# Performance work log

Hardware: AMD Instinct MI355X
Metric: run time of the kernel (lower is better)

The kernel has to match this reference:

```python
import jax, jax.numpy as jnp
import numpy as np

DIM = 1024
HEADS = 16
HEAD_DIM = DIM // HEADS


def rotate_half(x):
    x1, x2 = jnp.split(x, 2, axis=-1)
    return jnp.concatenate((-x2, x1), axis=-1)


def rope_tables(T, D, dtype=jnp.float32):
    inv_freq = 1.0 / (10000.0 ** (jnp.arange(0, D, 2, dtype=jnp.float32) / D))
    t = jnp.arange(T, dtype=jnp.float32)
    freqs = jnp.einsum('i,j->ij', t, inv_freq)  # [T, D/2]
    emb = jnp.concatenate((freqs, freqs), axis=-1)  # [T, D]
    return emb.astype(dtype), jnp.cos(emb).astype(dtype), jnp.sin(emb).astype(dtype)


def setup_inputs() -> dict:
    key = jax.random.key(0)
    kx, kq, kk, kv, ko = jax.random.split(key, 5)
    B, T = 2, 4096
    scale = 1.0 / np.sqrt(DIM)
    x = jax.random.normal(kx, (B, T, DIM), dtype=jnp.float32)
    wq = jax.random.normal(kq, (DIM, DIM), dtype=jnp.float32) * scale
    wk = jax.random.normal(kk, (DIM, DIM), dtype=jnp.float32) * scale
    wv = jax.random.normal(kv, (DIM, DIM), dtype=jnp.float32) * scale
    wo = jax.random.normal(ko, (DIM, DIM), dtype=jnp.float32) * scale
    return {"x": x, "wq": wq, "wk": wk, "wv": wv, "wo": wo}


def reference(x, wq, wk, wv, wo):
    B, T, C = x.shape
    H, D = HEADS, HEAD_DIM
    # projections; nn.Linear applies x @ W^T
    q = (x @ wq.T).reshape(B, T, H, D).transpose(0, 2, 1, 3)  # [B,H,T,D]
    k = (x @ wk.T).reshape(B, T, H, D).transpose(0, 2, 1, 3)
    v = (x @ wv.T).reshape(B, T, H, D).transpose(0, 2, 1, 3)
    _, cos, sin = rope_tables(T, D, x.dtype)
    cos = cos[None, None]  # [1,1,T,D]
    sin = sin[None, None]
    q = q * cos + rotate_half(q) * sin
    k = k * cos + rotate_half(k) * sin
    scores = jnp.einsum('bhtd,bhsd->bhts', q, k) / jnp.sqrt(jnp.asarray(D, x.dtype))
    attn = jax.nn.softmax(scores, axis=-1)
    out = jnp.einsum('bhts,bhsd->bhtd', attn, v)
    out = out.transpose(0, 2, 1, 3).reshape(B, T, C)
    return out @ wo.T
```

## Files before the change

### kernel.cpp

```cpp
#include <hip/hip_runtime.h>
#include <hip/hip_bf16.h>
#include <math.h>


typedef __attribute__((ext_vector_type(8))) short short8;
typedef __attribute__((ext_vector_type(4))) short short4v;
typedef __attribute__((ext_vector_type(4))) float floatx4;

using bf16 = __hip_bfloat16;

static constexpr int T_ = 4096;
static constexpr int C_ = 1024;
static constexpr int M_ = 8192;
static constexpr float QSCALE = 0.125f * 1.44269504088896340736f;

#if __has_builtin(__builtin_amdgcn_mfma_f32_16x16x16bf16_1k)
#define USE_K16 1
#else
#define USE_K16 0
#endif

#if __has_builtin(__builtin_amdgcn_exp2f)
#define EXP2 __builtin_amdgcn_exp2f
#else
#define EXP2 exp2f
#endif

__device__ __forceinline__ floatx4 mfma16(short8 a, short8 b, floatx4 c) {
    return __builtin_amdgcn_mfma_f32_16x16x32_bf16(a, b, c, 0, 0, 0);
}
#if USE_K16
__device__ __forceinline__ floatx4 mfma_k16(short4v a, short4v b, floatx4 c) {
    return __builtin_amdgcn_mfma_f32_16x16x16bf16_1k(a, b, c, 0, 0, 0);
}
#endif

__device__ __forceinline__ short8 ld8(const bf16* p) {
    return *reinterpret_cast<const short8*>(p);
}
__device__ __forceinline__ short4v ld4(const bf16* p) {
    return *reinterpret_cast<const short4v*>(p);
}
__device__ __forceinline__ void st8(bf16* p, short8 v) {
    *reinterpret_cast<short8*>(p) = v;
}
__device__ __forceinline__ unsigned short f2bf(float x) {
    bf16 h = __float2bfloat16(x);
    return reinterpret_cast<unsigned short&>(h);
}

__device__ __forceinline__ int pack2bf(float a, float b) {
    const unsigned ua = (__float_as_uint(a) + 0x8000u) >> 16;
    const unsigned ub = (__float_as_uint(b) + 0x8000u) & 0xFFFF0000u;
    return (int)(ua | ub);
}
__device__ __forceinline__ short4v i2s4(int lo, int hi) {
    union { int2 i; short4v s; } u;
    u.i.x = lo; u.i.y = hi;
    return u.s;
}

__device__ __forceinline__ void cp16(const bf16* g, bf16* l) {
    __builtin_amdgcn_global_load_lds(
        (const __attribute__((address_space(1))) void*)g,
        (__attribute__((address_space(3))) void*)l, 16, 0, 0);
}

__global__ __launch_bounds__(256)
void cvt_kernel(const float* __restrict__ in, bf16* __restrict__ out, int n8) {
    const int i = blockIdx.x * blockDim.x + threadIdx.x;
    if (i >= n8) return;
    const float4* p = reinterpret_cast<const float4*>(in) + (size_t)i * 2;
    const float4 a = p[0];
    const float4 b = p[1];
    short8 v;
    v[0] = (short)f2bf(a.x); v[1] = (short)f2bf(a.y);
    v[2] = (short)f2bf(a.z); v[3] = (short)f2bf(a.w);
    v[4] = (short)f2bf(b.x); v[5] = (short)f2bf(b.y);
    v[6] = (short)f2bf(b.z); v[7] = (short)f2bf(b.w);
    *(reinterpret_cast<short8*>(out) + i) = v;
}

__global__ __launch_bounds__(256)
void gemm128_kernel(const bf16* __restrict__ A, const bf16* __restrict__ W,
                    void* __restrict__ out, int mode) {
    const int m0   = blockIdx.x * 128;
    const int n0   = blockIdx.y * 128;
    const int tid  = threadIdx.x;
    const int lane = tid & 63;
    const int wave = tid >> 6;
    const int quad = lane >> 4;
    const int lr   = lane & 15;
    const int wr   = (wave >> 1) * 64;
    const int wc   = (wave & 1) * 64;

    __shared__ __align__(16) bf16 Als[2][128 * 32];
    __shared__ __align__(16) bf16 Bls[2][128 * 32];

    const int srow = tid >> 2;
    const int scol = (tid & 3) * 8;

    floatx4 acc[4][4];
#pragma unroll
    for (int i = 0; i < 4; ++i)
#pragma unroll
        for (int j = 0; j < 4; ++j) acc[i][j] = floatx4{0.f, 0.f, 0.f, 0.f};

    const bf16* Ab = A + (size_t)m0 * C_;
    const bf16* Wb = W + (size_t)n0 * C_;

#pragma unroll
    for (int j = 0; j < 2; ++j) {
        const int row = srow + j * 64;
        cp16(Ab + (size_t)row * C_ + scol, &Als[0][(j * 256 + tid) * 8]);
        cp16(Wb + (size_t)row * C_ + scol, &Bls[0][(j * 256 + tid) * 8]);
    }
    __syncthreads();

    for (int k = 0; k < C_; k += 32) {
        const int buf = (k >> 5) & 1;
        if (k + 32 < C_) {
            const int nb = buf ^ 1;
#pragma unroll
            for (int j = 0; j < 2; ++j) {
                const int row = srow + j * 64;
                cp16(Ab + (size_t)row * C_ + k + 32 + scol,
                     &Als[nb][(j * 256 + tid) * 8]);
                cp16(Wb + (size_t)row * C_ + k + 32 + scol,
                     &Bls[nb][(j * 256 + tid) * 8]);
            }
        }

        short8 a[4], b[4];
#pragma unroll
        for (int i = 0; i < 4; ++i)
            a[i] = ld8(&Als[buf][(wr + i * 16 + lr) * 32 + quad * 8]);
#pragma unroll
        for (int j = 0; j < 4; ++j)
            b[j] = ld8(&Bls[buf][(wc + j * 16 + lr) * 32 + quad * 8]);
#pragma unroll
        for (int i = 0; i < 4; ++i)
#pragma unroll
            for (int j = 0; j < 4; ++j) acc[i][j] = mfma16(a[i], b[j], acc[i][j]);

        __syncthreads();
    }

    if (mode == 0) {
        bf16* ob = (bf16*)out;
#pragma unroll
        for (int j = 0; j < 4; ++j) {
            const int col = n0 + wc + j * 16 + lr;
#pragma unroll
            for (int i = 0; i < 4; ++i)
#pragma unroll
                for (int r = 0; r < 4; ++r) {
                    const int m = m0 + wr + i * 16 + quad * 4 + r;
                    ob[(size_t)m * C_ + col] = __float2bfloat16(acc[i][j][r]);
                }
        }
    } else if (mode == 1) {
        unsigned short* ob = (unsigned short*)out;
        const int b2 = m0 >> 12;
#pragma unroll
        for (int j = 0; j < 4; ++j) {
            const int n = n0 + wc + j * 16 + lr;
            const int h = n >> 6;
            const int d = n & 63;
#pragma unroll
            for (int i = 0; i < 4; ++i) {
                const int t0 = (m0 & 4095) + wr + i * 16 + quad * 4;
                ushort4 v;
                v.x = f2bf(acc[i][j][0]); v.y = f2bf(acc[i][j][1]);
                v.z = f2bf(acc[i][j][2]); v.w = f2bf(acc[i][j][3]);
                size_t idx = ((size_t)((b2 * 16 + h) * 64 + d)) * T_ + t0;
                *reinterpret_cast<ushort4*>(ob + idx) = v;
            }
        }
    } else {
        float* of = (float*)out;
#pragma unroll
        for (int j = 0; j < 4; ++j) {
            const int col = n0 + wc + j * 16 + lr;
#pragma unroll
            for (int i = 0; i < 4; ++i)
#pragma unroll
                for (int r = 0; r < 4; ++r) {
                    const int m = m0 + wr + i * 16 + quad * 4 + r;
                    of[(size_t)m * C_ + col] = acc[i][j][r];
                }
        }
    }
}

__global__ __launch_bounds__(256)
void rope_kernel(bf16* __restrict__ Q, bf16* __restrict__ K) {
    const int tid  = blockIdx.x * blockDim.x + threadIdx.x;
    const int m    = tid >> 9;
    const int rest = tid & 511;
    const int h    = rest >> 5;
    const int j    = rest & 31;
    const int t    = m & 4095;

    const float inv_freq = expf(-(float)j * 0.28782313662425575f);
    const float angle = (float)t * inv_freq;
    float s, c;
    sincosf(angle, &s, &c);

    const size_t base = (size_t)m * C_ + h * 64 + j;

    float q1 = __bfloat162float(Q[base]);
    float q2 = __bfloat162float(Q[base + 32]);
    Q[base]      = __float2bfloat16((q1 * c - q2 * s) * QSCALE);
    Q[base + 32] = __float2bfloat16((q2 * c + q1 * s) * QSCALE);

    float k1 = __bfloat162float(K[base]);
    float k2 = __bfloat162float(K[base + 32]);
    K[base]      = __float2bfloat16(k1 * c - k2 * s);
    K[base + 32] = __float2bfloat16(k2 * c + k1 * s);
}

__global__ __launch_bounds__(256)
void attn_kernel(const bf16* __restrict__ Q, const bf16* __restrict__ K,
                 const bf16* __restrict__ Vt, bf16* __restrict__ AO) {
    const int tid  = threadIdx.x;
    const int lane = tid & 63;
    const int wave = tid >> 6;
    const int quad = lane >> 4;
    const int lr   = lane & 15;
    const int bh   = blockIdx.y;
    const int b    = bh >> 4;
    const int h    = bh & 15;
    const int q0   = blockIdx.x * 128 + wave * 32;

    const bf16* Qb = Q + (size_t)b * T_ * C_ + h * 64;
    const bf16* Kb = K + (size_t)b * T_ * C_ + h * 64;
    const bf16* Vb = Vt + (size_t)bh * 64 * T_;

#if USE_K16
    __shared__ __align__(16) bf16 Kls[2][64 * 64];
    __shared__ __align__(16) bf16 Vls[2][64 * 64];

    const int srow  = tid >> 3;
    const int sc    = tid & 7;
    const int sphys = (sc ^ (srow & 7)) * 8;
    const int soff0 = srow * 64 + sphys;
    const int soff1 = (srow + 32) * 64 + sphys;

    short8 aq[2][2];
#pragma unroll
    for (int t = 0; t < 2; ++t) {
        aq[t][0] = ld8(Qb + (size_t)(q0 + t * 16 + lr) * C_ + quad * 8);
        aq[t][1] = ld8(Qb + (size_t)(q0 + t * 16 + lr) * C_ + 32 + quad * 8);
    }

    floatx4 O[2][4];
#pragma unroll
    for (int t = 0; t < 2; ++t)
#pragma unroll
        for (int dt = 0; dt < 4; ++dt) O[t][dt] = floatx4{0.f, 0.f, 0.f, 0.f};
    float lsum[2] = {0.f, 0.f};

    short8 kr0, kr1, vr0, vr1;
#define LOAD_STAGE(kv0)                                              \
    do {                                                             \
        kr0 = ld8(Kb + (size_t)((kv0) + srow) * C_ + sc * 8);        \
        kr1 = ld8(Kb + (size_t)((kv0) + srow + 32) * C_ + sc * 8);   \
        vr0 = ld8(Vb + (size_t)srow * T_ + (kv0) + sc * 8);          \
        vr1 = ld8(Vb + (size_t)(srow + 32) * T_ + (kv0) + sc * 8);   \
    } while (0)
#define STORE_STAGE(p)                                               \
    do {                                                             \
        st8(&Kls[p][soff0], kr0);                                    \
        st8(&Kls[p][soff1], kr1);                                    \
        st8(&Vls[p][soff0], vr0);                                    \
        st8(&Vls[p][soff1], vr1);                                    \
    } while (0)

    LOAD_STAGE(0);
    STORE_STAGE(0);
    LOAD_STAGE(64);
    __syncthreads();

    const int lr7    = lr & 7;
    const int kchunk = (quad ^ lr7) * 8;
    const int vsub   = (quad & 1) * 4;
    const int vbq    = quad >> 1;

    constexpr int NS = T_ / 64;
    for (int s = 0; s < NS; ++s) {
        if (s + 1 < NS) STORE_STAGE((s + 1) & 1);
        if (s + 2 < NS) LOAD_STAGE((s + 2) * 64);

        const bf16* Ks = Kls[s & 1];
        const bf16* Vs = Vls[s & 1];

        int prlo[2][4], prhi[2][4];
        float rs0 = 0.f, rs1 = 0.f;
#pragma unroll
        for (int kk = 0; kk < 4; ++kk) {
            const int ka = (kk * 16 + lr) * 64 + kchunk;
            const short8 kf0 = ld8(Ks + ka);
            const short8 kf1 = ld8(Ks + (ka ^ 32));

            floatx4 s0 = {0.f, 0.f, 0.f, 0.f};
            s0 = mfma16(kf0, aq[0][0], s0);
            s0 = mfma16(kf1, aq[0][1], s0);
            floatx4 s1 = {0.f, 0.f, 0.f, 0.f};
            s1 = mfma16(kf0, aq[1][0], s1);
            s1 = mfma16(kf1, aq[1][1], s1);

            const float e0 = EXP2(s0[0]), e1 = EXP2(s0[1]);
            const float e2 = EXP2(s0[2]), e3 = EXP2(s0[3]);
            rs0 += (e0 + e1) + (e2 + e3);
            prlo[0][kk] = pack2bf(e0, e1);
            prhi[0][kk] = pack2bf(e2, e3);

            const float f0 = EXP2(s1[0]), f1 = EXP2(s1[1]);
            const float f2 = EXP2(s1[2]), f3 = EXP2(s1[3]);
            rs1 += (f0 + f1) + (f2 + f3);
            prlo[1][kk] = pack2bf(f0, f1);
            prhi[1][kk] = pack2bf(f2, f3);
        }
        lsum[0] += rs0;
        lsum[1] += rs1;

#pragma unroll
        for (int dt = 0; dt < 4; ++dt) {
            const int vrow = (dt * 16 + lr) * 64;
#pragma unroll
            for (int kk = 0; kk < 4; ++kk) {
                const int phys = ((2 * kk + vbq) ^ lr7) * 8;
                const short4v vf = ld4(Vs + vrow + phys + vsub);
                O[0][dt] = mfma_k16(i2s4(prlo[0][kk], prhi[0][kk]), vf, O[0][dt]);
                O[1][dt] = mfma_k16(i2s4(prlo[1][kk], prhi[1][kk]), vf, O[1][dt]);
            }
        }
        __syncthreads();
    }

#pragma unroll
    for (int t = 0; t < 2; ++t) {
        lsum[t] += __shfl_xor(lsum[t], 16);
        lsum[t] += __shfl_xor(lsum[t], 32);
    }

#pragma unroll
    for (int t = 0; t < 2; ++t) {
#pragma unroll
        for (int r = 0; r < 4; ++r) {
            const float lrow = __shfl(lsum[t], quad * 4 + r);
            const float inv = 1.0f / fmaxf(lrow, 1e-30f);
            const size_t row =
                (size_t)(b * T_ + q0 + t * 16 + quad * 4 + r) * C_ + h * 64;
            AO[row + 0  + lr] = __float2bfloat16(O[t][0][r] * inv);
            AO[row + 16 + lr] = __float2bfloat16(O[t][1][r] * inv);
            AO[row + 32 + lr] = __float2bfloat16(O[t][2][r] * inv);
            AO[row + 48 + lr] = __float2bfloat16(O[t][3][r] * inv);
        }
    }
#undef LOAD_STAGE
#undef STORE_STAGE
#else
    __shared__ __align__(16) unsigned short Pbuf[4][512];
    unsigned short* Pw = Pbuf[wave];
    for (int half = 0; half < 2; ++half) {
        const int qh = q0 + half * 16;
        const short8 aq0 = ld8(Qb + (size_t)(qh + lr) * C_ + quad * 8);
        const short8 aq1 = ld8(Qb + (size_t)(qh + lr) * C_ + 32 + quad * 8);
        floatx4 O0 = {0,0,0,0}, O1 = {0,0,0,0}, O2 = {0,0,0,0}, O3 = {0,0,0,0};
        float lrun[4] = {0.f, 0.f, 0.f, 0.f};
        for (int kv = 0; kv < T_; kv += 32) {
            floatx4 S0 = {0,0,0,0}, S1 = {0,0,0,0};
            const bf16* k0 = Kb + (size_t)(kv + lr) * C_ + quad * 8;
            const bf16* k1 = Kb + (size_t)(kv + 16 + lr) * C_ + quad * 8;
            S0 = mfma16(aq0, ld8(k0), S0);
            S0 = mfma16(aq1, ld8(k0 + 32), S0);
            S1 = mfma16(aq0, ld8(k1), S1);
            S1 = mfma16(aq1, ld8(k1 + 32), S1);
#pragma unroll
            for (int r = 0; r < 4; ++r) {
                const float e0 = exp2f(S0[r]);
                const float e1 = exp2f(S1[r]);
                lrun[r] += e0 + e1;
                const int row = quad * 4 + r;
                Pw[row * 32 + lr]      = f2bf(e0);
                Pw[row * 32 + 16 + lr] = f2bf(e1);
            }
            __syncthreads();
            const short8 ap = *reinterpret_cast<const short8*>(Pw + lr * 32 + quad * 8);
            O0 = mfma16(ap, ld8(Vb + (size_t)(lr)      * T_ + kv + quad * 8), O0);
            O1 = mfma16(ap, ld8(Vb + (size_t)(16 + lr) * T_ + kv + quad * 8), O1);
            O2 = mfma16(ap, ld8(Vb + (size_t)(32 + lr) * T_ + kv + quad * 8), O2);
            O3 = mfma16(ap, ld8(Vb + (size_t)(48 + lr) * T_ + kv + quad * 8), O3);
            __syncthreads();
        }
#pragma unroll
        for (int r = 0; r < 4; ++r) {
            float l = lrun[r];
            l += __shfl_xor(l, 1); l += __shfl_xor(l, 2);
            l += __shfl_xor(l, 4); l += __shfl_xor(l, 8);
            const float inv = 1.0f / fmaxf(l, 1e-30f);
            const size_t row = (size_t)(b * T_ + qh + quad * 4 + r) * C_ + h * 64;
            AO[row + 0  + lr] = __float2bfloat16(O0[r] * inv);
            AO[row + 16 + lr] = __float2bfloat16(O1[r] * inv);
            AO[row + 32 + lr] = __float2bfloat16(O2[r] * inv);
            AO[row + 48 + lr] = __float2bfloat16(O3[r] * inv);
        }
    }
#endif
}

extern "C" void kernel_launch(void* const* d_in, const int* in_sizes, int n_in,
                              void* d_out, int out_size, void* d_ws, size_t ws_size,
                              hipStream_t stream) {
    const float* x  = (const float*)d_in[0];
    const float* wq = (const float*)d_in[1];
    const float* wk = (const float*)d_in[2];
    const float* wv = (const float*)d_in[3];
    const float* wo = (const float*)d_in[4];
    float* out = (float*)d_out;

    bf16* xb  = (bf16*)d_ws;
    bf16* wqb = xb  + (size_t)M_ * C_;
    bf16* wkb = wqb + (size_t)C_ * C_;
    bf16* wvb = wkb + (size_t)C_ * C_;
    bf16* wob = wvb + (size_t)C_ * C_;
    bf16* Q   = wob + (size_t)C_ * C_;
    bf16* K   = Q   + (size_t)M_ * C_;
    bf16* Vt  = K   + (size_t)M_ * C_;
    bf16* AO  = xb;

    cvt_kernel<<<(M_ * C_ / 8 + 255) / 256, 256, 0, stream>>>(x, xb, M_ * C_ / 8);
    cvt_kernel<<<(C_ * C_ / 8 + 255) / 256, 256, 0, stream>>>(wq, wqb, C_ * C_ / 8);
    cvt_kernel<<<(C_ * C_ / 8 + 255) / 256, 256, 0, stream>>>(wk, wkb, C_ * C_ / 8);
    cvt_kernel<<<(C_ * C_ / 8 + 255) / 256, 256, 0, stream>>>(wv, wvb, C_ * C_ / 8);
    cvt_kernel<<<(C_ * C_ / 8 + 255) / 256, 256, 0, stream>>>(wo, wob, C_ * C_ / 8);

    const dim3 gg(M_ / 128, C_ / 128);
    const dim3 gb(256);

    gemm128_kernel<<<gg, gb, 0, stream>>>(xb, wqb, Q, 0);
    gemm128_kernel<<<gg, gb, 0, stream>>>(xb, wkb, K, 0);
    gemm128_kernel<<<gg, gb, 0, stream>>>(xb, wvb, Vt, 1);

    rope_kernel<<<(M_ * 512) / 256, 256, 0, stream>>>(Q, K);

    attn_kernel<<<dim3(T_ / 128, 32), 256, 0, stream>>>(Q, K, Vt, AO);

    gemm128_kernel<<<gg, gb, 0, stream>>>(AO, wob, out, 2);
}
```

Measured before the change: 436.9 us.

## Fuse QKV GEMMs into one launch; unroll attention loop and pack via v_perm

Replaces the three separate Q/K/V projection GEMM launches with a single fused kernel over a 24-column-block grid. It relies on wq/wk/wv and Q/K/Vt being laid out contiguously in the workspace, and the V segment is written transposed. The attention main loop is manually unrolled by two with fixed LDS buffer indices, and LDS offsets are precomputed. The bf16 packing of probabilities now uses a single v_perm_b32. The aim is to cut launch overhead, improve GPU fill and shave ALU and index-math work in the hot loop, at the cost of larger code and reliance on that buffer adjacency.

```diff
diff --git a/kernel.cpp b/kernel.cpp
--- a/kernel.cpp
+++ b/kernel.cpp
@@ -49,10 +49,12 @@
     return reinterpret_cast<unsigned short&>(h);
 }
 
-__device__ __forceinline__ int pack2bf(float a, float b) {
-    const unsigned ua = (__float_as_uint(a) + 0x8000u) >> 16;
-    const unsigned ub = (__float_as_uint(b) + 0x8000u) & 0xFFFF0000u;
-    return (int)(ua | ub);
+__device__ __forceinline__ int pack2bf(float a, float b, unsigned sel) {
+    const unsigned ua = __float_as_uint(a) + 0x8000u;
+    const unsigned ub = __float_as_uint(b) + 0x8000u;
+    int r;
+    asm("v_perm_b32 %0, %1, %2, %3" : "=v"(r) : "v"(ub), "v"(ua), "s"(sel));
+    return r;
 }
 __device__ __forceinline__ short4v i2s4(int lo, int hi) {
     union { int2 i; short4v s; } u;
@@ -194,6 +196,107 @@
 }
 
 __global__ __launch_bounds__(256)
+void gemm_qkv_kernel(const bf16* __restrict__ A, const bf16* __restrict__ W,
+                     bf16* __restrict__ Qbase) {
+    const int m0   = blockIdx.x * 128;
+    const int n0g  = blockIdx.y * 128;
+    const int tid  = threadIdx.x;
+    const int lane = tid & 63;
+    const int wave = tid >> 6;
+    const int quad = lane >> 4;
+    const int lr   = lane & 15;
+    const int wr   = (wave >> 1) * 64;
+    const int wc   = (wave & 1) * 64;
+
+    __shared__ __align__(16) bf16 Als[2][128 * 32];
+    __shared__ __align__(16) bf16 Bls[2][128 * 32];
+
+    const int srow = tid >> 2;
+    const int scol = (tid & 3) * 8;
+
+    floatx4 acc[4][4];
+#pragma unroll
+    for (int i = 0; i < 4; ++i)
+#pragma unroll
+        for (int j = 0; j < 4; ++j) acc[i][j] = floatx4{0.f, 0.f, 0.f, 0.f};
+
+    const bf16* Ab = A + (size_t)m0 * C_;
+    const bf16* Wb = W + (size_t)n0g * C_;
+
+#pragma unroll
+    for (int j = 0; j < 2; ++j) {
+        const int row = srow + j * 64;
+        cp16(Ab + (size_t)row * C_ + scol, &Als[0][(j * 256 + tid) * 8]);
+        cp16(Wb + (size_t)row * C_ + scol, &Bls[0][(j * 256 + tid) * 8]);
+    }
+    __syncthreads();
+
+    for (int k = 0; k < C_; k += 32) {
+        const int buf = (k >> 5) & 1;
+        if (k + 32 < C_) {
+            const int nb = buf ^ 1;
+#pragma unroll
+            for (int j = 0; j < 2; ++j) {
+                const int row = srow + j * 64;
+                cp16(Ab + (size_t)row * C_ + k + 32 + scol,
+                     &Als[nb][(j * 256 + tid) * 8]);
+                cp16(Wb + (size_t)row * C_ + k + 32 + scol,
+                     &Bls[nb][(j * 256 + tid) * 8]);
+            }
+        }
+
+        short8 a[4], b[4];
+#pragma unroll
+        for (int i = 0; i < 4; ++i)
+            a[i] = ld8(&Als[buf][(wr + i * 16 + lr) * 32 + quad * 8]);
+#pragma unroll
+        for (int j = 0; j < 4; ++j)
+            b[j] = ld8(&Bls[buf][(wc + j * 16 + lr) * 32 + quad * 8]);
+#pragma unroll
+        for (int i = 0; i < 4; ++i)
+#pragma unroll
+            for (int j = 0; j < 4; ++j) acc[i][j] = mfma16(a[i], b[j], acc[i][j]);
+
+        __syncthreads();
+    }
+
+    const int seg = n0g >> 10;
+    const int n0  = n0g & 1023;
+    if (seg < 2) {
+        bf16* ob = Qbase + (size_t)seg * M_ * C_;
+#pragma unroll
+        for (int j = 0; j < 4; ++j) {
+            const int col = n0 + wc + j * 16 + lr;
+#pragma unroll
+            for (int i = 0; i < 4; ++i)
+#pragma unroll
+                for (int r = 0; r < 4; ++r) {
+                    const int m = m0 + wr + i * 16 + quad * 4 + r;
+                    ob[(size_t)m * C_ + col] = __float2bfloat16(acc[i][j][r]);
+                }
+        }
+    } else {
+        unsigned short* ob = (unsigned short*)(Qbase + (size_t)2 * M_ * C_);
+        const int b2 = m0 >> 12;
+#pragma unroll
+        for (int j = 0; j < 4; ++j) {
+            const int n = n0 + wc + j * 16 + lr;
+            const int h = n >> 6;
+            const int d = n & 63;
+#pragma unroll
+            for (int i = 0; i < 4; ++i) {
+                const int t0 = (m0 & 4095) + wr + i * 16 + quad * 4;
+                ushort4 v;
+                v.x = f2bf(acc[i][j][0]); v.y = f2bf(acc[i][j][1]);
+                v.z = f2bf(acc[i][j][2]); v.w = f2bf(acc[i][j][3]);
+                size_t idx = ((size_t)((b2 * 16 + h) * 64 + d)) * T_ + t0;
+                *reinterpret_cast<ushort4*>(ob + idx) = v;
+            }
+        }
+    }
+}
+
+__global__ __launch_bounds__(256)
 void rope_kernel(bf16* __restrict__ Q, bf16* __restrict__ K) {
     const int tid  = blockIdx.x * blockDim.x + threadIdx.x;
     const int m    = tid >> 9;
@@ -247,6 +350,8 @@
     const int soff0 = srow * 64 + sphys;
     const int soff1 = (srow + 32) * 64 + sphys;
 
+    const unsigned psel = 0x07060302u;
+
     short8 aq[2][2];
 #pragma unroll
     for (int t = 0; t < 2; ++t) {
@@ -260,6 +365,17 @@
 #pragma unroll
         for (int dt = 0; dt < 4; ++dt) O[t][dt] = floatx4{0.f, 0.f, 0.f, 0.f};
     float lsum[2] = {0.f, 0.f};
+
+    const int lr7    = lr & 7;
+    const int kchunk = (quad ^ lr7) * 8;
+    const int vsub   = (quad & 1) * 4;
+    const int vbq    = quad >> 1;
+    const int kel0   = lr * 64 + kchunk;
+    const int kel1   = kel0 ^ 32;
+    int velk[4];
+#pragma unroll
+    for (int kk = 0; kk < 4; ++kk)
+        velk[kk] = lr * 64 + (((2 * kk + vbq) ^ lr7) * 8) + vsub;
 
     short8 kr0, kr1, vr0, vr1;
 #define LOAD_STAGE(kv0)                                              \
@@ -277,65 +393,60 @@
         st8(&Vls[p][soff1], vr1);                                    \
     } while (0)
 
+#define COMPUTE(P)                                                            \
+    do {                                                                      \
+        const bf16* Ks = Kls[P];                                              \
+        const bf16* Vs = Vls[P];                                              \
+        int prlo[2][4], prhi[2][4];                                           \
+        float rs0 = 0.f, rs1 = 0.f;                                           \
+        _Pragma("unroll")                                                     \
+        for (int kk = 0; kk < 4; ++kk) {                                      \
+            const short8 kf0 = ld8(Ks + kk * 1024 + kel0);                    \
+            const short8 kf1 = ld8(Ks + kk * 1024 + kel1);                    \
+            floatx4 s0 = {0.f, 0.f, 0.f, 0.f};                                \
+            s0 = mfma16(kf0, aq[0][0], s0);                                   \
+            s0 = mfma16(kf1, aq[0][1], s0);                                   \
+            floatx4 s1 = {0.f, 0.f, 0.f, 0.f};                                \
+            s1 = mfma16(kf0, aq[1][0], s1);                                   \
+            s1 = mfma16(kf1, aq[1][1], s1);                                   \
+            const float e0 = EXP2(s0[0]), e1 = EXP2(s0[1]);                   \
+            const float e2 = EXP2(s0[2]), e3 = EXP2(s0[3]);                   \
+            rs0 += (e0 + e1) + (e2 + e3);                                     \
+            prlo[0][kk] = pack2bf(e0, e1, psel);                              \
+            prhi[0][kk] = pack2bf(e2, e3, psel);                              \
+            const float f0 = EXP2(s1[0]), f1 = EXP2(s1[1]);                   \
+            const float f2 = EXP2(s1[2]), f3 = EXP2(s1[3]);                   \
+            rs1 += (f0 + f1) + (f2 + f3);                                     \
+            prlo[1][kk] = pack2bf(f0, f1, psel);                              \
+            prhi[1][kk] = pack2bf(f2, f3, psel);                              \
+        }                                                                     \
+        lsum[0] += rs0;                                                       \
+        lsum[1] += rs1;                                                       \
+        _Pragma("unroll")                                                     \
+        for (int dt = 0; dt < 4; ++dt) {                                      \
+            _Pragma("unroll")                                                 \
+            for (int kk = 0; kk < 4; ++kk) {                                  \
+                const short4v vf = ld4(Vs + dt * 1024 + velk[kk]);            \
+                O[0][dt] = mfma_k16(i2s4(prlo[0][kk], prhi[0][kk]), vf, O[0][dt]); \
+                O[1][dt] = mfma_k16(i2s4(prlo[1][kk], prhi[1][kk]), vf, O[1][dt]); \
+            }                                                                 \
+        }                                                                     \
+    } while (0)
+
     LOAD_STAGE(0);
     STORE_STAGE(0);
     LOAD_STAGE(64);
     __syncthreads();
 
-    const int lr7    = lr & 7;
-    const int kchunk = (quad ^ lr7) * 8;
-    const int vsub   = (quad & 1) * 4;
-    const int vbq    = quad >> 1;
-
     constexpr int NS = T_ / 64;
-    for (int s = 0; s < NS; ++s) {
-        if (s + 1 < NS) STORE_STAGE((s + 1) & 1);
+    for (int s = 0; s < NS; s += 2) {
+        if (s + 1 < NS) STORE_STAGE(1);
         if (s + 2 < NS) LOAD_STAGE((s + 2) * 64);
-
-        const bf16* Ks = Kls[s & 1];
-        const bf16* Vs = Vls[s & 1];
-
-        int prlo[2][4], prhi[2][4];
-        float rs0 = 0.f, rs1 = 0.f;
-#pragma unroll
-        for (int kk = 0; kk < 4; ++kk) {
-            const int ka = (kk * 16 + lr) * 64 + kchunk;
-            const short8 kf0 = ld8(Ks + ka);
-            const short8 kf1 = ld8(Ks + (ka ^ 32));
-
-            floatx4 s0 = {0.f, 0.f, 0.f, 0.f};
-            s0 = mfma16(kf0, aq[0][0], s0);
-            s0 = mfma16(kf1, aq[0][1], s0);
-            floatx4 s1 = {0.f, 0.f, 0.f, 0.f};
-            s1 = mfma16(kf0, aq[1][0], s1);
-            s1 = mfma16(kf1, aq[1][1], s1);
-
-            const float e0 = EXP2(s0[0]), e1 = EXP2(s0[1]);
-            const float e2 = EXP2(s0[2]), e3 = EXP2(s0[3]);
-            rs0 += (e0 + e1) + (e2 + e3);
-            prlo[0][kk] = pack2bf(e0, e1);
-            prhi[0][kk] = pack2bf(e2, e3);
-
-            const float f0 = EXP2(s1[0]), f1 = EXP2(s1[1]);
-            const float f2 = EXP2(s1[2]), f3 = EXP2(s1[3]);
-            rs1 += (f0 + f1) + (f2 + f3);
-            prlo[1][kk] = pack2bf(f0, f1);
-            prhi[1][kk] = pack2bf(f2, f3);
-        }
-        lsum[0] += rs0;
-        lsum[1] += rs1;
-
-#pragma unroll
-        for (int dt = 0; dt < 4; ++dt) {
-            const int vrow = (dt * 16 + lr) * 64;
-#pragma unroll
-            for (int kk = 0; kk < 4; ++kk) {
-                const int phys = ((2 * kk + vbq) ^ lr7) * 8;
-                const short4v vf = ld4(Vs + vrow + phys + vsub);
-                O[0][dt] = mfma_k16(i2s4(prlo[0][kk], prhi[0][kk]), vf, O[0][dt]);
-                O[1][dt] = mfma_k16(i2s4(prlo[1][kk], prhi[1][kk]), vf, O[1][dt]);
-            }
-        }
+        COMPUTE(0);
+        __syncthreads();
+        if (s + 2 < NS) STORE_STAGE(0);
+        if (s + 3 < NS) LOAD_STAGE((s + 3) * 64);
+        COMPUTE(1);
         __syncthreads();
     }
 
@@ -361,6 +472,7 @@
     }
 #undef LOAD_STAGE
 #undef STORE_STAGE
+#undef COMPUTE
 #else
     __shared__ __align__(16) unsigned short Pbuf[4][512];
     unsigned short* Pw = Pbuf[wave];
@@ -437,16 +549,11 @@
     cvt_kernel<<<(C_ * C_ / 8 + 255) / 256, 256, 0, stream>>>(wv, wvb, C_ * C_ / 8);
     cvt_kernel<<<(C_ * C_ / 8 + 255) / 256, 256, 0, stream>>>(wo, wob, C_ * C_ / 8);
 
-    const dim3 gg(M_ / 128, C_ / 128);
-    const dim3 gb(256);
-
-    gemm128_kernel<<<gg, gb, 0, stream>>>(xb, wqb, Q, 0);
-    gemm128_kernel<<<gg, gb, 0, stream>>>(xb, wkb, K, 0);
-    gemm128_kernel<<<gg, gb, 0, stream>>>(xb, wvb, Vt, 1);
+    gemm_qkv_kernel<<<dim3(M_ / 128, 24), dim3(256), 0, stream>>>(xb, wqb, Q);
 
     rope_kernel<<<(M_ * 512) / 256, 256, 0, stream>>>(Q, K);
 
     attn_kernel<<<dim3(T_ / 128, 32), 256, 0, stream>>>(Q, K, Vt, AO);
 
-    gemm128_kernel<<<gg, gb, 0, stream>>>(AO, wob, out, 2);
-}
+    gemm128_kernel<<<dim3(M_ / 128, C_ / 128), dim3(256), 0, stream>>>(AO, wob, out, 2);
+}
```

Measured after the change: 387.4 us. 11.3% less time.
